# Kernel optimization log

Hardware: AMD Instinct MI355X
Metric: run time of the kernel (lower is better)

The kernel has to match this reference:

```python
import jax, jax.numpy as jnp
import numpy as np

N = 1_000_000      # particles
K = 27             # 3x3x3 stencil taps
C_IN = 16
C_OUT = 4
NSTENCILS = 3


def setup_inputs() -> dict:
    key = jax.random.key(0)
    k1, k2, k3, k4 = jax.random.split(key, 4)
    x = jax.random.normal(k1, (N, C_IN), dtype=jnp.float32)
    W = jax.random.normal(k2, (NSTENCILS, K, C_IN, C_OUT), dtype=jnp.float32) * (1.0 / np.sqrt(K * C_IN))
    aprs = jax.random.randint(k3, (N, K), 0, N, dtype=jnp.int64)
    level_deltas = jax.random.randint(k4, (N,), 0, NSTENCILS, dtype=jnp.int64)
    return {"x": x, "W": W, "aprs": aprs, "level_deltas": level_deltas}


def reference(x, W, aprs, level_deltas):
    # Irregular neighbor gather: [N, K, C_in]
    gathered = x[aprs]
    # Level-dependent stencil contraction + select (nstencils is tiny, loop is over stencils not data)
    out = jnp.zeros((x.shape[0], W.shape[-1]), dtype=x.dtype)
    for s in range(NSTENCILS):
        contrib = jnp.einsum('nkc,kcd->nd', gathered, W[s])  # [N, C_out]
        out = jnp.where((level_deltas == s)[:, None], contrib, out)
    # Unfused final activation (nn.ReLU in OutBlock)
    return jax.nn.relu(out)
```

## Files before the change

### kernel.cpp

```cpp
#include <hip/hip_runtime.h>

constexpr int K    = 27;
constexpr int CIN  = 16;
constexpr int COUT = 4;
constexpr int NS   = 3;
constexpr int WSZ  = K * CIN * COUT;
constexpr int WPAD = WSZ + 8;

constexpr int NCH  = 16;
constexpr int CHSH = 16;
constexpr int NPL  = 4;
constexpr int NPW  = 256;
constexpr int RNDS = K * NPL;
constexpr int EPW  = RNDS * 64;
constexpr unsigned int SENT = 0xFFFFFFFFu;
constexpr int WREG = 34;

typedef unsigned int uint;
typedef float  f32x4 __attribute__((ext_vector_type(4)));
typedef uint   u32x4 __attribute__((ext_vector_type(4)));
typedef uint   u32x2 __attribute__((ext_vector_type(2)));

__device__ __forceinline__ uint bf16_rne(float f) {
    uint u = __float_as_uint(f);
    u += 0x7FFFu + ((u >> 16) & 1u);
    return u >> 16;
}
__device__ __forceinline__ float blo(uint u) { return __uint_as_float(u << 16); }
__device__ __forceinline__ float bhi(uint u) { return __uint_as_float(u & 0xFFFF0000u); }

__global__ __launch_bounds__(256) void cvt_kernel(
    const float* __restrict__ x, uint* __restrict__ xh, int nvec)
{
    int i = blockIdx.x * 256 + threadIdx.x;
    if (i >= nvec) return;
    const f32x4* xf = reinterpret_cast<const f32x4*>(x) + 2 * (size_t)i;
    f32x4 a = __builtin_nontemporal_load(&xf[0]);
    f32x4 b = __builtin_nontemporal_load(&xf[1]);
    u32x4 o;
    o.x = bf16_rne(a.x) | (bf16_rne(a.y) << 16);
    o.y = bf16_rne(a.z) | (bf16_rne(a.w) << 16);
    o.z = bf16_rne(b.x) | (bf16_rne(b.y) << 16);
    o.w = bf16_rne(b.z) | (bf16_rne(b.w) << 16);
    __builtin_nontemporal_store(o, &reinterpret_cast<u32x4*>(xh)[i]);
}

__global__ __launch_bounds__(64) void bucket_kernel(
    const int* __restrict__ aprs,
    const int* __restrict__ lvl,
    uint* __restrict__ ent,
    int n)
{
    __shared__ uint stage[EPW];
    __shared__ int  posL[NCH * 64];

    const int w    = blockIdx.x;
    const int lane = threadIdx.x;
    const int i0   = w * NPW + lane * NPL;
    const int* __restrict__ ap = aprs + (size_t)i0 * K;

    #pragma unroll
    for (int c = 0; c < NCH; ++c) posL[c * 64 + lane] = 0;
    for (int t = 0; t < RNDS; ++t) stage[t * 64 + lane] = SENT;

    for (int b = 0; b < NPL; ++b) {
        if (i0 + b < n) {
            for (int j = 0; j < K; ++j) {
                const int ch = (int)(((uint)ap[b * K + j]) >> CHSH);
                posL[ch * 64 + lane] += 1;
            }
        }
    }
    int run = 0;
    #pragma unroll
    for (int c = 0; c < NCH; ++c) {
        const int cc = posL[c * 64 + lane];
        posL[c * 64 + lane] = run;
        run += cc;
    }
    for (int b = 0; b < NPL; ++b) {
        if (i0 + b < n) {
            const uint s = (uint)lvl[i0 + b];
            const uint tag = ((uint)b << 7) | (s << 5);
            for (int j = 0; j < K; ++j) {
                const uint nb = (uint)ap[b * K + j];
                const int ch  = (int)(nb >> CHSH);
                const int slot = posL[ch * 64 + lane];
                posL[ch * 64 + lane] = slot + 1;
                stage[slot * 64 + lane] = (nb << 9) | tag | (uint)j;
            }
        }
    }
    uint* __restrict__ eb = ent + (size_t)w * EPW;
    for (int t = 0; t < RNDS; ++t) eb[t * 64 + lane] = stage[t * 64 + lane];
}

__global__ __launch_bounds__(256, 4) void compute_kernel(
    const uint*  __restrict__ xh,
    const float* __restrict__ Wg,
    const uint*  __restrict__ ent,
    float*       __restrict__ out,
    int n)
{
    __shared__ __align__(8) uint Wb[NS * K * WREG];

    const int tid = threadIdx.x;
    for (int idx = tid; idx < NS * K * 32; idx += 256) {
        const int region = idx >> 5, g = idx & 31;
        Wb[region * WREG + g] =
            bf16_rne(Wg[region * 64 + 2 * g]) | (bf16_rne(Wg[region * 64 + 2 * g + 1]) << 16);
    }
    __syncthreads();

    const int widx = tid >> 6, lane = tid & 63;
    const int w = blockIdx.x * 4 + widx;
    const uint* __restrict__ eb = ent + (size_t)w * EPW;

    f32x4 A0 = {0,0,0,0}, A1 = {0,0,0,0}, A2 = {0,0,0,0}, A3 = {0,0,0,0};

    uint eC = eb[lane];
    uint eN = eb[64 + lane];
    {
        const uint nbC = (eC == SENT) ? 0u : (eC >> 9);
        const u32x4* __restrict__ xr =
            reinterpret_cast<const u32x4*>(xh + (size_t)nbC * 8);
        u32x4 xC0 = xr[0];
        u32x4 xC1 = xr[1];

        for (int s = 0; s < RNDS; ++s) {
            const int sF = (s + 2 < RNDS) ? s + 2 : RNDS - 1;
            const uint eF = eb[sF * 64 + lane];
            const uint nbN = (eN == SENT) ? 0u : (eN >> 9);
            const u32x4* __restrict__ xrN =
                reinterpret_cast<const u32x4*>(xh + (size_t)nbN * 8);
            const u32x4 xN0 = xrN[0];
            const u32x4 xN1 = xrN[1];

            const bool valid = (eC != SENT);
            const uint bq = valid ? ((eC >> 7) & 3u) : 4u;
            const uint sk = valid ? (((eC >> 5) & 3u) * (uint)K + (eC & 31u)) : 0u;
            const uint* __restrict__ wr = &Wb[sk * WREG];

            uint xd[8];
            xd[0] = xC0.x; xd[1] = xC0.y; xd[2] = xC0.z; xd[3] = xC0.w;
            xd[4] = xC1.x; xd[5] = xC1.y; xd[6] = xC1.z; xd[7] = xC1.w;

            float a0 = 0.f, a1 = 0.f, a2 = 0.f, a3 = 0.f;
            #pragma unroll
            for (int cc = 0; cc < CIN; ++cc) {
                const u32x2 wv = *reinterpret_cast<const u32x2*>(wr + cc * 2);
                const float xc = (cc & 1) ? bhi(xd[cc >> 1]) : blo(xd[cc >> 1]);
                a0 = fmaf(xc, blo(wv.x), a0);
                a1 = fmaf(xc, bhi(wv.x), a1);
                a2 = fmaf(xc, blo(wv.y), a2);
                a3 = fmaf(xc, bhi(wv.y), a3);
            }
            const float m0 = (bq == 0u) ? 1.f : 0.f;
            const float m1 = (bq == 1u) ? 1.f : 0.f;
            const float m2 = (bq == 2u) ? 1.f : 0.f;
            const float m3 = (bq == 3u) ? 1.f : 0.f;
            A0.x = fmaf(m0, a0, A0.x); A0.y = fmaf(m0, a1, A0.y);
            A0.z = fmaf(m0, a2, A0.z); A0.w = fmaf(m0, a3, A0.w);
            A1.x = fmaf(m1, a0, A1.x); A1.y = fmaf(m1, a1, A1.y);
            A1.z = fmaf(m1, a2, A1.z); A1.w = fmaf(m1, a3, A1.w);
            A2.x = fmaf(m2, a0, A2.x); A2.y = fmaf(m2, a1, A2.y);
            A2.z = fmaf(m2, a2, A2.z); A2.w = fmaf(m2, a3, A2.w);
            A3.x = fmaf(m3, a0, A3.x); A3.y = fmaf(m3, a1, A3.y);
            A3.z = fmaf(m3, a2, A3.z); A3.w = fmaf(m3, a3, A3.w);

            eC = eN; xC0 = xN0; xC1 = xN1; eN = eF;
        }
    }

    const int i0 = w * NPW + lane * NPL;
    f32x4* __restrict__ op = reinterpret_cast<f32x4*>(out);
    f32x4 o;
    if (i0 + 0 < n) {
        o.x = fmaxf(A0.x,0.f); o.y = fmaxf(A0.y,0.f); o.z = fmaxf(A0.z,0.f); o.w = fmaxf(A0.w,0.f);
        __builtin_nontemporal_store(o, op + i0 + 0);
    }
    if (i0 + 1 < n) {
        o.x = fmaxf(A1.x,0.f); o.y = fmaxf(A1.y,0.f); o.z = fmaxf(A1.z,0.f); o.w = fmaxf(A1.w,0.f);
        __builtin_nontemporal_store(o, op + i0 + 1);
    }
    if (i0 + 2 < n) {
        o.x = fmaxf(A2.x,0.f); o.y = fmaxf(A2.y,0.f); o.z = fmaxf(A2.z,0.f); o.w = fmaxf(A2.w,0.f);
        __builtin_nontemporal_store(o, op + i0 + 2);
    }
    if (i0 + 3 < n) {
        o.x = fmaxf(A3.x,0.f); o.y = fmaxf(A3.y,0.f); o.z = fmaxf(A3.z,0.f); o.w = fmaxf(A3.w,0.f);
        __builtin_nontemporal_store(o, op + i0 + 3);
    }
}

__global__ __launch_bounds__(256) void outblock_bf16(
    const uint*  __restrict__ xh,
    const float* __restrict__ W,
    const int*   __restrict__ aprs,
    const int*   __restrict__ lvl,
    float*       __restrict__ out,
    int n)
{
    __shared__ float Wl[NS * WPAD];
    for (int i = threadIdx.x; i < NS * WSZ; i += 256) {
        int s = i / WSZ;
        Wl[s * WPAD + (i - s * WSZ)] = W[i];
    }
    __syncthreads();

    int nIdx = blockIdx.x * 256 + threadIdx.x;
    if (nIdx >= n) return;

    const int s = lvl[nIdx];
    const float* __restrict__ Ws = &Wl[s * WPAD];
    const int*   __restrict__ ap = aprs + (size_t)nIdx * K;

    float a0 = 0.f, a1 = 0.f, a2 = 0.f, a3 = 0.f;
    #pragma unroll 3
    for (int k = 0; k < K; ++k) {
        const int nb = ap[k];
        const u32x4* __restrict__ xr =
            reinterpret_cast<const u32x4*>(xh + (size_t)nb * 8);
        const u32x4 p0 = xr[0];
        const u32x4 p1 = xr[1];
        const float* __restrict__ Wk = Ws + k * (CIN * COUT);
        float xv[16];
        xv[ 0] = blo(p0.x); xv[ 1] = bhi(p0.x);
        xv[ 2] = blo(p0.y); xv[ 3] = bhi(p0.y);
        xv[ 4] = blo(p0.z); xv[ 5] = bhi(p0.z);
        xv[ 6] = blo(p0.w); xv[ 7] = bhi(p0.w);
        xv[ 8] = blo(p1.x); xv[ 9] = bhi(p1.x);
        xv[10] = blo(p1.y); xv[11] = bhi(p1.y);
        xv[12] = blo(p1.z); xv[13] = bhi(p1.z);
        xv[14] = blo(p1.w); xv[15] = bhi(p1.w);
        #pragma unroll
        for (int cq = 0; cq < CIN; ++cq) {
            const float4 wv = *reinterpret_cast<const float4*>(&Wk[cq * COUT]);
            a0 = fmaf(xv[cq], wv.x, a0);
            a1 = fmaf(xv[cq], wv.y, a1);
            a2 = fmaf(xv[cq], wv.z, a2);
            a3 = fmaf(xv[cq], wv.w, a3);
        }
    }
    f32x4 o;
    o.x = fmaxf(a0, 0.f); o.y = fmaxf(a1, 0.f);
    o.z = fmaxf(a2, 0.f); o.w = fmaxf(a3, 0.f);
    __builtin_nontemporal_store(o, reinterpret_cast<f32x4*>(out) + nIdx);
}

__global__ __launch_bounds__(256) void outblock_f32(
    const float* __restrict__ x,
    const float* __restrict__ W,
    const int*   __restrict__ aprs,
    const int*   __restrict__ lvl,
    float*       __restrict__ out,
    int n)
{
    __shared__ float Wl[NS * WPAD];
    for (int i = threadIdx.x; i < NS * WSZ; i += 256) {
        int s = i / WSZ;
        Wl[s * WPAD + (i - s * WSZ)] = W[i];
    }
    __syncthreads();
    int nIdx = blockIdx.x * 256 + threadIdx.x;
    if (nIdx >= n) return;
    const int s = lvl[nIdx];
    const float* __restrict__ Ws = &Wl[s * WPAD];
    const int*   __restrict__ ap = aprs + (size_t)nIdx * K;
    float a0 = 0.f, a1 = 0.f, a2 = 0.f, a3 = 0.f;
    #pragma unroll 3
    for (int k = 0; k < K; ++k) {
        const int nb = ap[k];
        const float4* __restrict__ xr =
            reinterpret_cast<const float4*>(x + (size_t)nb * CIN);
        const float4 v0 = xr[0], v1 = xr[1], v2 = xr[2], v3 = xr[3];
        const float* __restrict__ Wk = Ws + k * (CIN * COUT);
        float xv[16];
        xv[ 0] = v0.x; xv[ 1] = v0.y; xv[ 2] = v0.z; xv[ 3] = v0.w;
        xv[ 4] = v1.x; xv[ 5] = v1.y; xv[ 6] = v1.z; xv[ 7] = v1.w;
        xv[ 8] = v2.x; xv[ 9] = v2.y; xv[10] = v2.z; xv[11] = v2.w;
        xv[12] = v3.x; xv[13] = v3.y; xv[14] = v3.z; xv[15] = v3.w;
        #pragma unroll
        for (int cq = 0; cq < CIN; ++cq) {
            const float4 wv = *reinterpret_cast<const float4*>(&Wk[cq * COUT]);
            a0 = fmaf(xv[cq], wv.x, a0);
            a1 = fmaf(xv[cq], wv.y, a1);
            a2 = fmaf(xv[cq], wv.z, a2);
            a3 = fmaf(xv[cq], wv.w, a3);
        }
    }
    float4 o;
    o.x = fmaxf(a0, 0.f); o.y = fmaxf(a1, 0.f);
    o.z = fmaxf(a2, 0.f); o.w = fmaxf(a3, 0.f);
    reinterpret_cast<float4*>(out)[nIdx] = o;
}

extern "C" void kernel_launch(void* const* d_in, const int* in_sizes, int n_in,
                              void* d_out, int out_size, void* d_ws, size_t ws_size,
                              hipStream_t stream) {
    const float* x    = (const float*)d_in[0];
    const float* W    = (const float*)d_in[1];
    const int*   aprs = (const int*)d_in[2];
    const int*   lvl  = (const int*)d_in[3];
    float*       out  = (float*)d_out;

    const int n = in_sizes[0] / CIN;

    const int nwaves = ((n + NPW - 1) / NPW + 3) & ~3;
    const int nblocks = nwaves / 4;

    const size_t xhB  = (size_t)n * CIN * 2;
    const size_t entB = (size_t)nwaves * EPW * 4;
    const size_t needChunked = xhB + entB;

    if (ws_size >= needChunked && n <= (1 << 20)) {
        uint* xh  = (uint*)d_ws;
        uint* ent = (uint*)((char*)d_ws + xhB);
        const int nvec = n * CIN / 8;
        cvt_kernel<<<(nvec + 255) / 256, 256, 0, stream>>>(x, xh, nvec);
        bucket_kernel<<<nwaves, 64, 0, stream>>>(aprs, lvl, ent, n);
        compute_kernel<<<nblocks, 256, 0, stream>>>(xh, W, ent, out, n);
    } else if (ws_size >= xhB) {
        uint* xh = (uint*)d_ws;
        const int nvec = n * CIN / 8;
        cvt_kernel<<<(nvec + 255) / 256, 256, 0, stream>>>(x, xh, nvec);
        outblock_bf16<<<(n + 255) / 256, 256, 0, stream>>>(xh, W, aprs, lvl, out, n);
    } else {
        outblock_f32<<<(n + 255) / 256, 256, 0, stream>>>(x, W, aprs, lvl, out, n);
    }
}
```

Measured before the change: 364.6 us.

## Switch gather to fp16 dot2 and sync waves per neighbor chunk

Converts x and W to fp16 instead of bf16, so the 16-wide contraction can use packed dot2 instructions (v_dot2_f32_f16) with a reshuffled weight layout. The compute kernel now uses 8-wave blocks, and all waves in a block walk the 16 neighbor-index chunks in lockstep, with a __syncthreads after each chunk. The aim is to keep the set of gathered x rows in cache (L2/MALL) small at any moment and to cut VALU work per entry. The cost is divergent while-loops, a barrier per chunk, and fp16 range and precision limits on the inputs.

```diff
diff --git a/kernel.cpp b/kernel.cpp
--- a/kernel.cpp
+++ b/kernel.cpp
@@ -15,11 +15,39 @@
 constexpr int EPW  = RNDS * 64;
 constexpr unsigned int SENT = 0xFFFFFFFFu;
 constexpr int WREG = 34;
+constexpr int BW   = 8;
+constexpr int TPB  = BW * 64;
 
 typedef unsigned int uint;
 typedef float  f32x4 __attribute__((ext_vector_type(4)));
 typedef uint   u32x4 __attribute__((ext_vector_type(4)));
 typedef uint   u32x2 __attribute__((ext_vector_type(2)));
+typedef _Float16 h16x2 __attribute__((ext_vector_type(2)));
+
+__device__ __forceinline__ uint pkh(float lo, float hi) {
+    union { h16x2 h; uint u; } v;
+    v.h.x = (_Float16)lo; v.h.y = (_Float16)hi;
+    return v.u;
+}
+__device__ __forceinline__ h16x2 u2h(uint u) {
+    union { uint u; h16x2 h; } v; v.u = u; return v.h;
+}
+
+#if defined(__has_builtin)
+#if __has_builtin(__builtin_amdgcn_fdot2)
+#define HAVE_FDOT2 1
+#endif
+#endif
+
+__device__ __forceinline__ float dot2acc(uint xp, uint wp, float acc) {
+#ifdef HAVE_FDOT2
+    return __builtin_amdgcn_fdot2(u2h(xp), u2h(wp), acc, false);
+#else
+    const h16x2 a = u2h(xp), b = u2h(wp);
+    acc = fmaf((float)a.x, (float)b.x, acc);
+    return fmaf((float)a.y, (float)b.y, acc);
+#endif
+}
 
 __device__ __forceinline__ uint bf16_rne(float f) {
     uint u = __float_as_uint(f);
@@ -29,7 +57,185 @@
 __device__ __forceinline__ float blo(uint u) { return __uint_as_float(u << 16); }
 __device__ __forceinline__ float bhi(uint u) { return __uint_as_float(u & 0xFFFF0000u); }
 
-__global__ __launch_bounds__(256) void cvt_kernel(
+__global__ __launch_bounds__(256) void cvt_f16(
+    const float* __restrict__ x, uint* __restrict__ xh, int nvec)
+{
+    int i = blockIdx.x * 256 + threadIdx.x;
+    if (i >= nvec) return;
+    const f32x4* xf = reinterpret_cast<const f32x4*>(x) + 2 * (size_t)i;
+    f32x4 a = __builtin_nontemporal_load(&xf[0]);
+    f32x4 b = __builtin_nontemporal_load(&xf[1]);
+    u32x4 o;
+    o.x = pkh(a.x, a.y);
+    o.y = pkh(a.z, a.w);
+    o.z = pkh(b.x, b.y);
+    o.w = pkh(b.z, b.w);
+    __builtin_nontemporal_store(o, &reinterpret_cast<u32x4*>(xh)[i]);
+}
+
+__global__ __launch_bounds__(64) void bucket_kernel(
+    const int* __restrict__ aprs,
+    const int* __restrict__ lvl,
+    uint* __restrict__ ent,
+    int n)
+{
+    __shared__ uint stage[EPW];
+    __shared__ int  posL[NCH * 64];
+
+    const int w    = blockIdx.x;
+    const int lane = threadIdx.x;
+    const int i0   = w * NPW + lane * NPL;
+    const int* __restrict__ ap = aprs + (size_t)i0 * K;
+
+    #pragma unroll
+    for (int c = 0; c < NCH; ++c) posL[c * 64 + lane] = 0;
+    for (int t = 0; t < RNDS; ++t) stage[t * 64 + lane] = SENT;
+
+    for (int b = 0; b < NPL; ++b) {
+        if (i0 + b < n) {
+            for (int j = 0; j < K; ++j) {
+                const int ch = (int)(((uint)ap[b * K + j]) >> CHSH);
+                posL[ch * 64 + lane] += 1;
+            }
+        }
+    }
+    int run = 0;
+    #pragma unroll
+    for (int c = 0; c < NCH; ++c) {
+        const int cc = posL[c * 64 + lane];
+        posL[c * 64 + lane] = run;
+        run += cc;
+    }
+    for (int b = 0; b < NPL; ++b) {
+        if (i0 + b < n) {
+            const uint s = (uint)lvl[i0 + b];
+            const uint tag = ((uint)b << 7) | (s << 5);
+            for (int j = 0; j < K; ++j) {
+                const uint nb = (uint)ap[b * K + j];
+                const int ch  = (int)(nb >> CHSH);
+                const int slot = posL[ch * 64 + lane];
+                posL[ch * 64 + lane] = slot + 1;
+                stage[slot * 64 + lane] = (nb << 9) | tag | (uint)j;
+            }
+        }
+    }
+    uint* __restrict__ eb = ent + (size_t)w * EPW;
+    for (int t = 0; t < RNDS; ++t) eb[t * 64 + lane] = stage[t * 64 + lane];
+}
+
+__global__ __launch_bounds__(TPB, 4) void compute_kernel(
+    const uint*  __restrict__ xh,
+    const float* __restrict__ Wg,
+    const uint*  __restrict__ ent,
+    float*       __restrict__ out,
+    int n)
+{
+    __shared__ __align__(8) uint Wb[NS * K * WREG];
+
+    const int tid = threadIdx.x;
+    for (int idx = tid; idx < NS * K * 32; idx += TPB) {
+        const int reg = idx >> 5, g = idx & 31;
+        const int q = g >> 3, p = g & 7;
+        Wb[reg * WREG + g] = pkh(Wg[reg * 64 + 8 * p + q],
+                                 Wg[reg * 64 + 8 * p + 4 + q]);
+    }
+    __syncthreads();
+
+    const int widx = tid >> 6, lane = tid & 63;
+    const int w = blockIdx.x * BW + widx;
+    const uint* __restrict__ eb = ent + (size_t)w * EPW;
+
+    f32x4 A0 = {0,0,0,0}, A1 = {0,0,0,0}, A2 = {0,0,0,0}, A3 = {0,0,0,0};
+
+    int  J  = 0;
+    uint eC = eb[lane];
+    uint eN = eb[64 + lane];
+    uint nbC = (eC == SENT) ? 0u : (eC >> 9);
+    const u32x4* __restrict__ xr0 = reinterpret_cast<const u32x4*>(xh + (size_t)nbC * 8);
+    u32x4 xC0 = xr0[0];
+    u32x4 xC1 = xr0[1];
+
+    for (int c = 0; c < NCH; ++c) {
+        bool act = (eC != SENT) && (J < RNDS) && ((eC >> (9 + CHSH)) == (uint)c);
+        while (__any(act ? 1 : 0)) {
+            const int sF = (J + 2 < RNDS) ? J + 2 : RNDS - 1;
+            const uint eF = eb[(size_t)sF * 64 + lane];
+            const uint nbN = (eN == SENT) ? 0u : (eN >> 9);
+            const u32x4* __restrict__ xrN =
+                reinterpret_cast<const u32x4*>(xh + (size_t)nbN * 8);
+            const u32x4 xN0 = xrN[0];
+            const u32x4 xN1 = xrN[1];
+
+            const uint bq  = (eC >> 7) & 3u;
+            const uint skr = ((eC >> 5) & 3u) * (uint)K + (eC & 31u);
+            const uint sk  = act ? skr : 0u;
+            const uint* __restrict__ wr = &Wb[sk * WREG];
+
+            uint xd[8];
+            xd[0] = xC0.x; xd[1] = xC0.y; xd[2] = xC0.z; xd[3] = xC0.w;
+            xd[4] = xC1.x; xd[5] = xC1.y; xd[6] = xC1.z; xd[7] = xC1.w;
+
+            float pq0 = 0.f, pq1 = 0.f, pq2 = 0.f, pq3 = 0.f;
+            #pragma unroll
+            for (int t = 0; t < 4; ++t) {
+                const u32x2 w0 = *reinterpret_cast<const u32x2*>(wr +  0 + 2 * t);
+                const u32x2 w1 = *reinterpret_cast<const u32x2*>(wr +  8 + 2 * t);
+                const u32x2 w2 = *reinterpret_cast<const u32x2*>(wr + 16 + 2 * t);
+                const u32x2 w3 = *reinterpret_cast<const u32x2*>(wr + 24 + 2 * t);
+                pq0 = dot2acc(xd[2 * t], w0.x, pq0);
+                pq0 = dot2acc(xd[2 * t + 1], w0.y, pq0);
+                pq1 = dot2acc(xd[2 * t], w1.x, pq1);
+                pq1 = dot2acc(xd[2 * t + 1], w1.y, pq1);
+                pq2 = dot2acc(xd[2 * t], w2.x, pq2);
+                pq2 = dot2acc(xd[2 * t + 1], w2.y, pq2);
+                pq3 = dot2acc(xd[2 * t], w3.x, pq3);
+                pq3 = dot2acc(xd[2 * t + 1], w3.y, pq3);
+            }
+            const float m0 = (act && bq == 0u) ? 1.f : 0.f;
+            const float m1 = (act && bq == 1u) ? 1.f : 0.f;
+            const float m2 = (act && bq == 2u) ? 1.f : 0.f;
+            const float m3 = (act && bq == 3u) ? 1.f : 0.f;
+            A0.x = fmaf(m0, pq0, A0.x); A0.y = fmaf(m0, pq1, A0.y);
+            A0.z = fmaf(m0, pq2, A0.z); A0.w = fmaf(m0, pq3, A0.w);
+            A1.x = fmaf(m1, pq0, A1.x); A1.y = fmaf(m1, pq1, A1.y);
+            A1.z = fmaf(m1, pq2, A1.z); A1.w = fmaf(m1, pq3, A1.w);
+            A2.x = fmaf(m2, pq0, A2.x); A2.y = fmaf(m2, pq1, A2.y);
+            A2.z = fmaf(m2, pq2, A2.z); A2.w = fmaf(m2, pq3, A2.w);
+            A3.x = fmaf(m3, pq0, A3.x); A3.y = fmaf(m3, pq1, A3.y);
+            A3.z = fmaf(m3, pq2, A3.z); A3.w = fmaf(m3, pq3, A3.w);
+
+            J  += act ? 1 : 0;
+            eC  = act ? eN : eC;
+            xC0 = act ? xN0 : xC0;
+            xC1 = act ? xN1 : xC1;
+            eN  = act ? eF : eN;
+            act = (eC != SENT) && (J < RNDS) && ((eC >> (9 + CHSH)) == (uint)c);
+        }
+        __syncthreads();
+    }
+
+    const int i0 = w * NPW + lane * NPL;
+    f32x4* __restrict__ op = reinterpret_cast<f32x4*>(out);
+    f32x4 o;
+    if (i0 + 0 < n) {
+        o.x = fmaxf(A0.x,0.f); o.y = fmaxf(A0.y,0.f); o.z = fmaxf(A0.z,0.f); o.w = fmaxf(A0.w,0.f);
+        __builtin_nontemporal_store(o, op + i0 + 0);
+    }
+    if (i0 + 1 < n) {
+        o.x = fmaxf(A1.x,0.f); o.y = fmaxf(A1.y,0.f); o.z = fmaxf(A1.z,0.f); o.w = fmaxf(A1.w,0.f);
+        __builtin_nontemporal_store(o, op + i0 + 1);
+    }
+    if (i0 + 2 < n) {
+        o.x = fmaxf(A2.x,0.f); o.y = fmaxf(A2.y,0.f); o.z = fmaxf(A2.z,0.f); o.w = fmaxf(A2.w,0.f);
+        __builtin_nontemporal_store(o, op + i0 + 2);
+    }
+    if (i0 + 3 < n) {
+        o.x = fmaxf(A3.x,0.f); o.y = fmaxf(A3.y,0.f); o.z = fmaxf(A3.z,0.f); o.w = fmaxf(A3.w,0.f);
+        __builtin_nontemporal_store(o, op + i0 + 3);
+    }
+}
+
+__global__ __launch_bounds__(256) void cvt_bf16(
     const float* __restrict__ x, uint* __restrict__ xh, int nvec)
 {
     int i = blockIdx.x * 256 + threadIdx.x;
@@ -43,154 +249,6 @@
     o.z = bf16_rne(b.x) | (bf16_rne(b.y) << 16);
     o.w = bf16_rne(b.z) | (bf16_rne(b.w) << 16);
     __builtin_nontemporal_store(o, &reinterpret_cast<u32x4*>(xh)[i]);
-}
-
-__global__ __launch_bounds__(64) void bucket_kernel(
-    const int* __restrict__ aprs,
-    const int* __restrict__ lvl,
-    uint* __restrict__ ent,
-    int n)
-{
-    __shared__ uint stage[EPW];
-    __shared__ int  posL[NCH * 64];
-
-    const int w    = blockIdx.x;
-    const int lane = threadIdx.x;
-    const int i0   = w * NPW + lane * NPL;
-    const int* __restrict__ ap = aprs + (size_t)i0 * K;
-
-    #pragma unroll
-    for (int c = 0; c < NCH; ++c) posL[c * 64 + lane] = 0;
-    for (int t = 0; t < RNDS; ++t) stage[t * 64 + lane] = SENT;
-
-    for (int b = 0; b < NPL; ++b) {
-        if (i0 + b < n) {
-            for (int j = 0; j < K; ++j) {
-                const int ch = (int)(((uint)ap[b * K + j]) >> CHSH);
-                posL[ch * 64 + lane] += 1;
-            }
-        }
-    }
-    int run = 0;
-    #pragma unroll
-    for (int c = 0; c < NCH; ++c) {
-        const int cc = posL[c * 64 + lane];
-        posL[c * 64 + lane] = run;
-        run += cc;
-    }
-    for (int b = 0; b < NPL; ++b) {
-        if (i0 + b < n) {
-            const uint s = (uint)lvl[i0 + b];
-            const uint tag = ((uint)b << 7) | (s << 5);
-            for (int j = 0; j < K; ++j) {
-                const uint nb = (uint)ap[b * K + j];
-                const int ch  = (int)(nb >> CHSH);
-                const int slot = posL[ch * 64 + lane];
-                posL[ch * 64 + lane] = slot + 1;
-                stage[slot * 64 + lane] = (nb << 9) | tag | (uint)j;
-            }
-        }
-    }
-    uint* __restrict__ eb = ent + (size_t)w * EPW;
-    for (int t = 0; t < RNDS; ++t) eb[t * 64 + lane] = stage[t * 64 + lane];
-}
-
-__global__ __launch_bounds__(256, 4) void compute_kernel(
-    const uint*  __restrict__ xh,
-    const float* __restrict__ Wg,
-    const uint*  __restrict__ ent,
-    float*       __restrict__ out,
-    int n)
-{
-    __shared__ __align__(8) uint Wb[NS * K * WREG];
-
-    const int tid = threadIdx.x;
-    for (int idx = tid; idx < NS * K * 32; idx += 256) {
-        const int region = idx >> 5, g = idx & 31;
-        Wb[region * WREG + g] =
-            bf16_rne(Wg[region * 64 + 2 * g]) | (bf16_rne(Wg[region * 64 + 2 * g + 1]) << 16);
-    }
-    __syncthreads();
-
-    const int widx = tid >> 6, lane = tid & 63;
-    const int w = blockIdx.x * 4 + widx;
-    const uint* __restrict__ eb = ent + (size_t)w * EPW;
-
-    f32x4 A0 = {0,0,0,0}, A1 = {0,0,0,0}, A2 = {0,0,0,0}, A3 = {0,0,0,0};
-
-    uint eC = eb[lane];
-    uint eN = eb[64 + lane];
-    {
-        const uint nbC = (eC == SENT) ? 0u : (eC >> 9);
-        const u32x4* __restrict__ xr =
-            reinterpret_cast<const u32x4*>(xh + (size_t)nbC * 8);
-        u32x4 xC0 = xr[0];
-        u32x4 xC1 = xr[1];
-
-        for (int s = 0; s < RNDS; ++s) {
-            const int sF = (s + 2 < RNDS) ? s + 2 : RNDS - 1;
-            const uint eF = eb[sF * 64 + lane];
-            const uint nbN = (eN == SENT) ? 0u : (eN >> 9);
-            const u32x4* __restrict__ xrN =
-                reinterpret_cast<const u32x4*>(xh + (size_t)nbN * 8);
-            const u32x4 xN0 = xrN[0];
-            const u32x4 xN1 = xrN[1];
-
-            const bool valid = (eC != SENT);
-            const uint bq = valid ? ((eC >> 7) & 3u) : 4u;
-            const uint sk = valid ? (((eC >> 5) & 3u) * (uint)K + (eC & 31u)) : 0u;
-            const uint* __restrict__ wr = &Wb[sk * WREG];
-
-            uint xd[8];
-            xd[0] = xC0.x; xd[1] = xC0.y; xd[2] = xC0.z; xd[3] = xC0.w;
-            xd[4] = xC1.x; xd[5] = xC1.y; xd[6] = xC1.z; xd[7] = xC1.w;
-
-            float a0 = 0.f, a1 = 0.f, a2 = 0.f, a3 = 0.f;
-            #pragma unroll
-            for (int cc = 0; cc < CIN; ++cc) {
-                const u32x2 wv = *reinterpret_cast<const u32x2*>(wr + cc * 2);
-                const float xc = (cc & 1) ? bhi(xd[cc >> 1]) : blo(xd[cc >> 1]);
-                a0 = fmaf(xc, blo(wv.x), a0);
-                a1 = fmaf(xc, bhi(wv.x), a1);
-                a2 = fmaf(xc, blo(wv.y), a2);
-                a3 = fmaf(xc, bhi(wv.y), a3);
-            }
-            const float m0 = (bq == 0u) ? 1.f : 0.f;
-            const float m1 = (bq == 1u) ? 1.f : 0.f;
-            const float m2 = (bq == 2u) ? 1.f : 0.f;
-            const float m3 = (bq == 3u) ? 1.f : 0.f;
-            A0.x = fmaf(m0, a0, A0.x); A0.y = fmaf(m0, a1, A0.y);
-            A0.z = fmaf(m0, a2, A0.z); A0.w = fmaf(m0, a3, A0.w);
-            A1.x = fmaf(m1, a0, A1.x); A1.y = fmaf(m1, a1, A1.y);
-            A1.z = fmaf(m1, a2, A1.z); A1.w = fmaf(m1, a3, A1.w);
-            A2.x = fmaf(m2, a0, A2.x); A2.y = fmaf(m2, a1, A2.y);
-            A2.z = fmaf(m2, a2, A2.z); A2.w = fmaf(m2, a3, A2.w);
-            A3.x = fmaf(m3, a0, A3.x); A3.y = fmaf(m3, a1, A3.y);
-            A3.z = fmaf(m3, a2, A3.z); A3.w = fmaf(m3, a3, A3.w);
-
-            eC = eN; xC0 = xN0; xC1 = xN1; eN = eF;
-        }
-    }
-
-    const int i0 = w * NPW + lane * NPL;
-    f32x4* __restrict__ op = reinterpret_cast<f32x4*>(out);
-    f32x4 o;
-    if (i0 + 0 < n) {
-        o.x = fmaxf(A0.x,0.f); o.y = fmaxf(A0.y,0.f); o.z = fmaxf(A0.z,0.f); o.w = fmaxf(A0.w,0.f);
-        __builtin_nontemporal_store(o, op + i0 + 0);
-    }
-    if (i0 + 1 < n) {
-        o.x = fmaxf(A1.x,0.f); o.y = fmaxf(A1.y,0.f); o.z = fmaxf(A1.z,0.f); o.w = fmaxf(A1.w,0.f);
-        __builtin_nontemporal_store(o, op + i0 + 1);
-    }
-    if (i0 + 2 < n) {
-        o.x = fmaxf(A2.x,0.f); o.y = fmaxf(A2.y,0.f); o.z = fmaxf(A2.z,0.f); o.w = fmaxf(A2.w,0.f);
-        __builtin_nontemporal_store(o, op + i0 + 2);
-    }
-    if (i0 + 3 < n) {
-        o.x = fmaxf(A3.x,0.f); o.y = fmaxf(A3.y,0.f); o.z = fmaxf(A3.z,0.f); o.w = fmaxf(A3.w,0.f);
-        __builtin_nontemporal_store(o, op + i0 + 3);
-    }
 }
 
 __global__ __launch_bounds__(256) void outblock_bf16(
@@ -306,24 +364,25 @@
 
     const int n = in_sizes[0] / CIN;
 
-    const int nwaves = ((n + NPW - 1) / NPW + 3) & ~3;
-    const int nblocks = nwaves / 4;
+    const int nwaves    = (n + NPW - 1) / NPW;
+    const int nblocks   = (nwaves + BW - 1) / BW;
+    const int nwavesPad = nblocks * BW;
 
     const size_t xhB  = (size_t)n * CIN * 2;
-    const size_t entB = (size_t)nwaves * EPW * 4;
+    const size_t entB = (size_t)nwavesPad * EPW * 4;
     const size_t needChunked = xhB + entB;
 
     if (ws_size >= needChunked && n <= (1 << 20)) {
         uint* xh  = (uint*)d_ws;
         uint* ent = (uint*)((char*)d_ws + xhB);
         const int nvec = n * CIN / 8;
-        cvt_kernel<<<(nvec + 255) / 256, 256, 0, stream>>>(x, xh, nvec);
-        bucket_kernel<<<nwaves, 64, 0, stream>>>(aprs, lvl, ent, n);
-        compute_kernel<<<nblocks, 256, 0, stream>>>(xh, W, ent, out, n);
+        cvt_f16<<<(nvec + 255) / 256, 256, 0, stream>>>(x, xh, nvec);
+        bucket_kernel<<<nwavesPad, 64, 0, stream>>>(aprs, lvl, ent, n);
+        compute_kernel<<<nblocks, TPB, 0, stream>>>(xh, W, ent, out, n);
     } else if (ws_size >= xhB) {
         uint* xh = (uint*)d_ws;
         const int nvec = n * CIN / 8;
-        cvt_kernel<<<(nvec + 255) / 256, 256, 0, stream>>>(x, xh, nvec);
+        cvt_bf16<<<(nvec + 255) / 256, 256, 0, stream>>>(x, xh, nvec);
         outblock_bf16<<<(n + 255) / 256, 256, 0, stream>>>(xh, W, aprs, lvl, out, n);
     } else {
         outblock_f32<<<(n + 255) / 256, 256, 0, stream>>>(x, W, aprs, lvl, out, n);
```

New measurement: 703.8 us. +93.0%, slower.
